# Kernel optimization log

Measured on AMD Instinct MI355X. Metric: run time of the kernel, lower is better.

Reference implementation:

```python
import jax, jax.numpy as jnp
import numpy as np
import math

LN_EPS = 1e-5
NORM_EPS = 1e-12


def _l2norm(v):
    # F.normalize(p=2, dim=-1): v / max(||v||, eps)
    n = jnp.sqrt(jnp.sum(v * v, axis=-1, keepdims=True))
    return v / jnp.maximum(n, NORM_EPS)


def setup_inputs() -> dict:
    key = jax.random.key(0)
    B, C, P, D, R = 64, 21, 96, 256, 32
    H = D // 4  # gate MLP hidden = 64
    ks = jax.random.split(key, 24)
    f32 = jnp.float32
    inp = {
        "x": jax.random.normal(ks[0], (B * C, P, D), dtype=f32),
        "ln_w": jnp.ones((D,), f32),
        "ln_b": jnp.zeros((D,), f32),
        "Wd": jax.random.normal(ks[1], (D, R), f32) / np.sqrt(D),
        "bd": jax.random.normal(ks[2], (R,), f32) * 0.02,
        "Wq": jax.random.normal(ks[3], (R, R), f32) / np.sqrt(R),
        "Wk": jax.random.normal(ks[4], (R, R), f32) / np.sqrt(R),
        "Wv": jax.random.normal(ks[5], (R, R), f32) / np.sqrt(R),
        "Wg": jax.random.normal(ks[6], (R, R), f32) / np.sqrt(R),
        "bg": jax.random.normal(ks[7], (R,), f32) * 0.02,
        "Wu": jax.random.normal(ks[8], (R, D), f32) / np.sqrt(R),
        "bu": jax.random.normal(ks[9], (D,), f32) * 0.02,
        "cn1_w": jax.random.normal(ks[10], (1, H), f32),
        "cn1_b": jax.random.normal(ks[11], (H,), f32) * 0.02,
        "cn2_w": jax.random.normal(ks[12], (H, D), f32) / np.sqrt(H),
        "cn2_b": jnp.full((D,), -5.0, f32),
        "dn1_w": jax.random.normal(ks[13], (D, H), f32) / np.sqrt(D),
        "dn1_b": jax.random.normal(ks[14], (H,), f32) * 0.02,
        "dn2_w": jax.random.normal(ks[15], (H, D), f32) / np.sqrt(H),
        "dn2_b": jax.random.normal(ks[16], (D,), f32) * 0.02,
        "epsilon": jnp.asarray(0.1, f32),
        "B": B,
        "C": C,
    }
    return inp


def reference(x, ln_w, ln_b, Wd, bd, Wq, Wk, Wv, Wg, bg, Wu, bu,
              cn1_w, cn1_b, cn2_w, cn2_b, dn1_w, dn1_b, dn2_w, dn2_b,
              epsilon, B, C):
    BC, P, D = x.shape
    gelu = lambda t: jax.nn.gelu(t, approximate=False)

    # [B*C,P,D] -> [B*P,C,D]: mix across channels per (batch, patch)
    h = x.reshape(B, C, P, D).transpose(0, 2, 1, 3).reshape(B * P, C, D)

    # LayerNorm over D
    mu = jnp.mean(h, axis=-1, keepdims=True)
    var = jnp.var(h, axis=-1, keepdims=True)
    h_norm = (h - mu) * jax.lax.rsqrt(var + LN_EPS) * ln_w + ln_b

    # bottleneck projection down to rank
    h_low = h_norm @ Wd + bd  # [BP, C, R]

    # Hydra attention: cosine-sim linear attention, global pool over C
    Q = _l2norm(h_low @ Wq)
    K = _l2norm(h_low @ Wk)
    V = h_low @ Wv
    global_feat = jnp.sum(K * V, axis=1, keepdims=True)  # [BP, 1, R]
    h_attn = Q * global_feat  # [BP, C, R]

    # content gate in low-rank space, then project up
    gate_c = jax.nn.sigmoid(h_low @ Wg + bg)
    mixed = (h_attn * gate_c) @ Wu + bu  # [BP, C, D]

    # AdaptiveGate (hybrid): channel MLP on log C + eps * data MLP on channel variance
    log_c = math.log(max(C, 2)) / math.log(1000.0)
    lc = jnp.full((1, 1), log_c, dtype=x.dtype)
    channel_logits = gelu(lc @ cn1_w + cn1_b) @ cn2_w + cn2_b  # [1, D]
    chan_var = jnp.var(h, axis=1, ddof=1)  # unbiased var over C -> [BP, D]
    data_corr = gelu(chan_var @ dn1_w + dn1_b) @ dn2_w + dn2_b  # [BP, D]
    gate_val = jax.nn.sigmoid(channel_logits + epsilon * data_corr)[:, None, :]

    out = h + gate_val * mixed  # [BP, C, D]
    return out.reshape(B, P, C, D).transpose(0, 2, 1, 3).reshape(BC, P, D)
```

## Files before the change

kernel.cpp:

```cpp
#include <hip/hip_runtime.h>
#include <math.h>


#define DD 256
#define CC 21
#define RR 32
#define HH 64
#define PP 96
#define BB 64
#define PD (PP * DD)
#define NBP (BB * PP)
#define NT 256

#define HBS 264
#define LWS 40

#define WS_WDB  0
#define WS_W4B  16384
#define WS_WUB  24576
#define WS_DN1P 40960
#define WS_DN2P 73728
#define WS_S1   106496
#define WS_S2   106624
#define WS_LG   106752

typedef __attribute__((ext_vector_type(8))) short bf16x8;
typedef __attribute__((ext_vector_type(4))) float f32x4;
typedef __attribute__((ext_vector_type(4))) unsigned short u16x4;

__device__ __forceinline__ float gelu_exact(float x) {
    return 0.5f * x * (1.0f + erff(x * 0.70710678118654752440f));
}
__device__ __forceinline__ float sigmoidf_(float x) {
    return 1.0f / (1.0f + __expf(-x));
}
__device__ __forceinline__ short f2bf(float f) {
    union { float f; unsigned u; } v; v.f = f;
    unsigned r = v.u + 0x7FFFu + ((v.u >> 16) & 1u);
    return (short)(unsigned short)(r >> 16);
}
__device__ __forceinline__ float bf2f_s(short s) {
    union { unsigned u; float f; } v; v.u = ((unsigned)(unsigned short)s) << 16;
    return v.f;
}

#define DPP_ADD(v, ctrl)                                                      \
    (v) += __builtin_bit_cast(float, __builtin_amdgcn_update_dpp(             \
               0, __builtin_bit_cast(int, (v)), (ctrl), 0xF, 0xF, true))

__device__ __forceinline__ float rowsum16(float v) {
    DPP_ADD(v, 0xB1);
    DPP_ADD(v, 0x4E);
    DPP_ADD(v, 0x124);
    DPP_ADD(v, 0x128);
    return v;
}
__device__ __forceinline__ float rdlane(float v, int l) {
    return __builtin_bit_cast(float,
        __builtin_amdgcn_readlane(__builtin_bit_cast(int, v), l));
}

extern "C" __global__ __launch_bounds__(NT)
void hydra_preproc(const float* __restrict__ ln_w, const float* __restrict__ ln_b,
                   const float* __restrict__ Wd,   const float* __restrict__ bd,
                   const float* __restrict__ Wq,   const float* __restrict__ Wk,
                   const float* __restrict__ Wv,   const float* __restrict__ Wg,
                   const float* __restrict__ Wu,
                   const float* __restrict__ cn1w, const float* __restrict__ cn1b,
                   const float* __restrict__ cn2w, const float* __restrict__ cn2b,
                   const float* __restrict__ dn1w, const float* __restrict__ dn2w,
                   short* __restrict__ WdB, short* __restrict__ W4B,
                   short* __restrict__ WuB, short* __restrict__ dn1P,
                   short* __restrict__ dn2P,
                   float* __restrict__ s1p, float* __restrict__ s2p,
                   float* __restrict__ logits)
{
    const int t = threadIdx.x, lane = t & 63, w = t >> 6, bid = blockIdx.x;
    const int q = lane >> 4, nl = lane & 15;

    if (bid < 4) {
        int tile = bid * 4 + w;
        int kb = tile >> 1, ni = tile & 1;
        int kbase = kb * 32 + q * 8;
        int n = ni * 16 + nl;
        bf16x8 o;
        #pragma unroll
        for (int j = 0; j < 8; ++j) {
            int k = kbase + j;
            o[j] = f2bf(ln_w[k] * Wd[k * RR + n]);
        }
        *(bf16x8*)(WdB + tile * 512 + lane * 8) = o;
    } else if (bid < 6) {
        int ni = (bid - 4) * 4 + w;
        int n = ni * 16 + nl;
        const float* Wsel = (n < 32) ? Wq : (n < 64) ? Wk : (n < 96) ? Wv : Wg;
        int nn = n & 31;
        bf16x8 o;
        #pragma unroll
        for (int j = 0; j < 8; ++j) o[j] = f2bf(Wsel[(q * 8 + j) * RR + nn]);
        *(bf16x8*)(W4B + ni * 512 + lane * 8) = o;
    } else if (bid < 10) {
        int ni = (bid - 6) * 4 + w;
        int n = ni * 16 + nl;
        bf16x8 o;
        #pragma unroll
        for (int j = 0; j < 8; ++j) o[j] = f2bf(Wu[(q * 8 + j) * DD + n]);
        *(bf16x8*)(WuB + ni * 512 + lane * 8) = o;
    } else if (bid == 10) {
        __shared__ float red1[8][33], red2[8][33];
        __shared__ float clh[HH];
        int r = t & 31, ks = t >> 5;
        float a1 = 0.f, a2 = 0.f;
        for (int k = ks * 32; k < ks * 32 + 32; ++k) {
            float wv = Wd[k * RR + r];
            a1 += bf2f_s(f2bf(ln_w[k] * wv));
            a2 += ln_b[k] * wv;
        }
        red1[ks][r] = a1; red2[ks][r] = a2;
        if (t < HH) {
            const float lc = 0.44073977f;
            clh[t] = gelu_exact(lc * cn1w[t] + cn1b[t]);
        }
        __syncthreads();
        if (t < RR) {
            float s1 = 0.f, s2 = 0.f;
            #pragma unroll
            for (int s = 0; s < 8; ++s) { s1 += red1[s][t]; s2 += red2[s][t]; }
            s1p[t] = s1;
            s2p[t] = s2 + bd[t];
        }
        float a = 0.f;
        #pragma unroll 8
        for (int j = 0; j < HH; ++j) a += clh[j] * cn2w[j * DD + t];
        logits[t] = a + cn2b[t];
    } else if (bid < 19) {
        int slot = (bid - 11) * 256 + t;
        int kb = slot >> 6, j = slot & 63;
        bf16x8 o;
        #pragma unroll
        for (int ki = 0; ki < 8; ++ki) o[ki] = f2bf(dn1w[(kb * 8 + ki) * HH + j]);
        *(bf16x8*)(dn1P + slot * 8) = o;
    } else {
        int slot = (bid - 19) * 256 + t;
        int jb = slot >> 8, d = slot & 255;
        bf16x8 o;
        #pragma unroll
        for (int ji = 0; ji < 8; ++ji) o[ji] = f2bf(dn2w[(jb * 8 + ji) * DD + d]);
        *(bf16x8*)(dn2P + slot * 8) = o;
    }
}

extern "C" __global__ __launch_bounds__(NT, 5)
void hydra_fused(const float* __restrict__ x,
                 const float* __restrict__ bg,   const float* __restrict__ bu,
                 const float* __restrict__ dn1b, const float* __restrict__ dn2b,
                 const float* __restrict__ eps_p,
                 const short* __restrict__ WdB,  const short* __restrict__ W4B,
                 const short* __restrict__ WuB,  const short* __restrict__ dn1P,
                 const short* __restrict__ dn2P,
                 const float* __restrict__ s1p,  const float* __restrict__ s2p,
                 const float* __restrict__ logits,
                 float* __restrict__ out)
{
    __shared__ __align__(16) short  hbf[CC * HBS];
    __shared__ __align__(16) short  lowbf[32 * LWS];
    __shared__ __align__(16) float  sh_cv[DD];
    __shared__ __align__(16) float2 murs[32];
    __shared__ __align__(16) float  dn1p[128];
    __shared__ __align__(16) float  sh_h1[HH];
    __shared__ __align__(16) float  gfp[64];
    __shared__ __align__(16) float  sh_gf[RR];
    __shared__ __align__(16) float  sh_gate[DD];

    const int t    = threadIdx.x;
    const int lane = t & 63;
    const int w    = t >> 6;
    const int quad = lane >> 4;
    const int nl   = lane & 15;
    const int bp = blockIdx.x;
    const int b  = bp / PP;
    const int p  = bp - b * PP;
    const float* xbase = x   + (size_t)b * CC * PD + (size_t)p * DD;
    float*       obase = out + (size_t)b * CC * PD + (size_t)p * DD;

    if (t >= 21 && t < 32) murs[t] = make_float2(0.f, 0.f);
    #pragma unroll
    for (int iter = 0; iter < 6; ++iter) {
        int c = iter * 4 + w;
        bool act = (c < CC);
        float4 v = make_float4(0.f, 0.f, 0.f, 0.f);
        if (act) v = *(const float4*)(xbase + (size_t)c * PD + lane * 4);
        if (act) {
            u16x4 u;
            u[0] = (unsigned short)f2bf(v.x); u[1] = (unsigned short)f2bf(v.y);
            u[2] = (unsigned short)f2bf(v.z); u[3] = (unsigned short)f2bf(v.w);
            *(u16x4*)(hbf + c * HBS + lane * 4) = u;
        }
        float s  = v.x + v.y + v.z + v.w;
        float s2 = v.x * v.x + v.y * v.y + v.z * v.z + v.w * v.w;
        s  = rowsum16(s);
        s2 = rowsum16(s2);
        float tot  = rdlane(s, 0)  + rdlane(s, 16)  + rdlane(s, 32)  + rdlane(s, 48);
        float tot2 = rdlane(s2, 0) + rdlane(s2, 16) + rdlane(s2, 32) + rdlane(s2, 48);
        if (act && lane == 0) {
            float mu  = tot * (1.0f / DD);
            float var = tot2 * (1.0f / DD) - mu * mu;
            murs[c] = make_float2(mu, rsqrtf(var + 1e-5f));
        }
    }
    __syncthreads();

    {
        float cs = 0.f, cs2 = 0.f;
        #pragma unroll
        for (int c = 0; c < CC; ++c) {
            float v = bf2f_s(hbf[c * HBS + t]);
            cs += v; cs2 += v * v;
        }
        sh_cv[t] = (cs2 - cs * cs * (1.0f / CC)) * (1.0f / (CC - 1));
    }
    {
        const int mi = w & 1, ni = w >> 1;
        const int m  = mi * 16 + nl;
        const int mc = (m < CC) ? m : (CC - 1);
        f32x4 acc = {0.f, 0.f, 0.f, 0.f};
        #pragma unroll
        for (int kb = 0; kb < 8; ++kb) {
            bf16x8 a  = *(const bf16x8*)(hbf + mc * HBS + kb * 32 + quad * 8);
            bf16x8 bw = *(const bf16x8*)(WdB + (kb * 2 + ni) * 512 + lane * 8);
            acc = __builtin_amdgcn_mfma_f32_16x16x32_bf16(a, bw, acc, 0, 0, 0);
        }
        const int colg = ni * 16 + nl;
        const float s1v = s1p[colg], s2v = s2p[colg];
        #pragma unroll
        for (int reg = 0; reg < 4; ++reg) {
            int rowg = mi * 16 + quad * 4 + reg;
            float2 mr = murs[rowg];
            float hl = mr.y * (acc[reg] - mr.x * s1v) + s2v;
            lowbf[rowg * LWS + colg] = f2bf(hl);
        }
    }
    __syncthreads();

    const int mi2 = w >> 1;
    float qg0[4], qg1[4];
    if ((w & 1) == 0) {
        const int m = mi2 * 16 + nl;
        bf16x8 a = *(const bf16x8*)(lowbf + m * LWS + quad * 8);
        f32x4 acc[8];
        #pragma unroll
        for (int i = 0; i < 8; ++i) {
            bf16x8 bw = *(const bf16x8*)(W4B + i * 512 + lane * 8);
            f32x4 z = {0.f, 0.f, 0.f, 0.f};
            acc[i] = __builtin_amdgcn_mfma_f32_16x16x32_bf16(a, bw, z, 0, 0, 0);
        }
        const float bg0 = bg[nl], bg1 = bg[16 + nl];
        float kv0 = 0.f, kv1 = 0.f;
        #pragma unroll
        for (int reg = 0; reg < 4; ++reg) {
            float q0 = acc[0][reg], q1 = acc[1][reg];
            float k0 = acc[2][reg], k1 = acc[3][reg];
            float q2 = rowsum16(q0 * q0 + q1 * q1);
            float k2 = rowsum16(k0 * k0 + k1 * k1);
            float qi = 1.0f / fmaxf(sqrtf(q2), 1e-12f);
            float ki = 1.0f / fmaxf(sqrtf(k2), 1e-12f);
            float g0 = sigmoidf_(acc[6][reg] + bg0);
            float g1 = sigmoidf_(acc[7][reg] + bg1);
            qg0[reg] = q0 * qi * g0;
            qg1[reg] = q1 * qi * g1;
            int rowg = mi2 * 16 + quad * 4 + reg;
            float msk = (rowg < CC) ? 1.0f : 0.0f;
            kv0 += msk * (k0 * ki * acc[4][reg]);
            kv1 += msk * (k1 * ki * acc[5][reg]);
        }
        kv0 += __shfl_xor(kv0, 16); kv0 += __shfl_xor(kv0, 32);
        kv1 += __shfl_xor(kv1, 16); kv1 += __shfl_xor(kv1, 32);
        if (quad == 0) {
            gfp[mi2 * 32 + nl]      = kv0;
            gfp[mi2 * 32 + 16 + nl] = kv1;
        }
    } else {
        const int half = w >> 1;
        float part = 0.f;
        #pragma unroll
        for (int i = 0; i < 16; ++i) {
            int kb = half * 16 + i;
            bf16x8 wv = *(const bf16x8*)(dn1P + (kb * 64 + lane) * 8);
            f32x4 c0 = *(const f32x4*)(sh_cv + kb * 8);
            f32x4 c1 = *(const f32x4*)(sh_cv + kb * 8 + 4);
            part += bf2f_s(wv[0]) * c0[0] + bf2f_s(wv[1]) * c0[1]
                  + bf2f_s(wv[2]) * c0[2] + bf2f_s(wv[3]) * c0[3]
                  + bf2f_s(wv[4]) * c1[0] + bf2f_s(wv[5]) * c1[1]
                  + bf2f_s(wv[6]) * c1[2] + bf2f_s(wv[7]) * c1[3];
        }
        dn1p[half * 64 + lane] = part;
    }
    __syncthreads();

    if (t < HH) sh_h1[t] = gelu_exact(dn1p[t] + dn1p[64 + t] + dn1b[t]);
    if (t < RR) sh_gf[t] = gfp[t] + gfp[32 + t];
    __syncthreads();

    {
        const float eps = eps_p[0];
        float a1 = 0.f;
        #pragma unroll
        for (int jb = 0; jb < 8; ++jb) {
            bf16x8 wv = *(const bf16x8*)(dn2P + (jb * 256 + t) * 8);
            f32x4 h0 = *(const f32x4*)(sh_h1 + jb * 8);
            f32x4 h1 = *(const f32x4*)(sh_h1 + jb * 8 + 4);
            a1 += bf2f_s(wv[0]) * h0[0] + bf2f_s(wv[1]) * h0[1]
                + bf2f_s(wv[2]) * h0[2] + bf2f_s(wv[3]) * h0[3]
                + bf2f_s(wv[4]) * h1[0] + bf2f_s(wv[5]) * h1[1]
                + bf2f_s(wv[6]) * h1[2] + bf2f_s(wv[7]) * h1[3];
        }
        sh_gate[t] = sigmoidf_(logits[t] + eps * (a1 + dn2b[t]));
    }
    if ((w & 1) == 0) {
        float gf0 = sh_gf[nl], gf1 = sh_gf[16 + nl];
        #pragma unroll
        for (int reg = 0; reg < 4; ++reg) {
            int rowg = mi2 * 16 + quad * 4 + reg;
            lowbf[rowg * LWS + nl]      = f2bf(qg0[reg] * gf0);
            lowbf[rowg * LWS + 16 + nl] = f2bf(qg1[reg] * gf1);
        }
    }
    __syncthreads();

    {
        const int mi = w & 1, nig = (w >> 1) * 8;
        const int m = mi * 16 + nl;
        bf16x8 a = *(const bf16x8*)(lowbf + m * LWS + quad * 8);
        #pragma unroll
        for (int i = 0; i < 8; ++i) {
            bf16x8 bw = *(const bf16x8*)(WuB + (nig + i) * 512 + lane * 8);
            f32x4 z = {0.f, 0.f, 0.f, 0.f};
            f32x4 acc = __builtin_amdgcn_mfma_f32_16x16x32_bf16(a, bw, z, 0, 0, 0);
            const int d   = (nig + i) * 16 + nl;
            const float gd  = sh_gate[d];
            const float bud = bu[d];
            #pragma unroll
            for (int reg = 0; reg < 4; ++reg) {
                int c = mi * 16 + quad * 4 + reg;
                if (c < CC) {
                    float hres = bf2f_s(hbf[c * HBS + d]);
                    obase[(size_t)c * PD + d] = hres + gd * (acc[reg] + bud);
                }
            }
        }
    }
}

extern "C" void kernel_launch(void* const* d_in, const int* in_sizes, int n_in,
                              void* d_out, int out_size, void* d_ws, size_t ws_size,
                              hipStream_t stream) {
    const float* x    = (const float*)d_in[0];
    const float* ln_w = (const float*)d_in[1];
    const float* ln_b = (const float*)d_in[2];
    const float* Wd   = (const float*)d_in[3];
    const float* bd   = (const float*)d_in[4];
    const float* Wq   = (const float*)d_in[5];
    const float* Wk   = (const float*)d_in[6];
    const float* Wv   = (const float*)d_in[7];
    const float* Wg   = (const float*)d_in[8];
    const float* bg   = (const float*)d_in[9];
    const float* Wu   = (const float*)d_in[10];
    const float* bu   = (const float*)d_in[11];
    const float* cn1w = (const float*)d_in[12];
    const float* cn1b = (const float*)d_in[13];
    const float* cn2w = (const float*)d_in[14];
    const float* cn2b = (const float*)d_in[15];
    const float* dn1w = (const float*)d_in[16];
    const float* dn1b = (const float*)d_in[17];
    const float* dn2w = (const float*)d_in[18];
    const float* dn2b = (const float*)d_in[19];
    const float* eps  = (const float*)d_in[20];
    float* out = (float*)d_out;

    char* ws = (char*)d_ws;
    short* WdB  = (short*)(ws + WS_WDB);
    short* W4B  = (short*)(ws + WS_W4B);
    short* WuB  = (short*)(ws + WS_WUB);
    short* dn1P = (short*)(ws + WS_DN1P);
    short* dn2P = (short*)(ws + WS_DN2P);
    float* s1p  = (float*)(ws + WS_S1);
    float* s2p  = (float*)(ws + WS_S2);
    float* lg   = (float*)(ws + WS_LG);

    hydra_preproc<<<27, NT, 0, stream>>>(ln_w, ln_b, Wd, bd, Wq, Wk, Wv, Wg, Wu,
                                         cn1w, cn1b, cn2w, cn2b, dn1w, dn2w,
                                         WdB, W4B, WuB, dn1P, dn2P, s1p, s2p, lg);
    hydra_fused<<<NBP, NT, 0, stream>>>(x, bg, bu, dn1b, dn2b, eps,
                                        WdB, W4B, WuB, dn1P, dn2P, s1p, s2p, lg,
                                        out);
}
```

Measured before the change: 350.6 us.

## Transpose MFMA operand roles so outputs write as contiguous vectorized float4 rows

Measured after the change: 323.5 us. 7.7% less time.

```diff
diff --git a/kernel.cpp b/kernel.cpp
--- a/kernel.cpp
+++ b/kernel.cpp
@@ -183,7 +183,6 @@
     const float* xbase = x   + (size_t)b * CC * PD + (size_t)p * DD;
     float*       obase = out + (size_t)b * CC * PD + (size_t)p * DD;
 
-    if (t >= 21 && t < 32) murs[t] = make_float2(0.f, 0.f);
     #pragma unroll
     for (int iter = 0; iter < 6; ++iter) {
         int c = iter * 4 + w;
@@ -215,30 +214,31 @@
         #pragma unroll
         for (int c = 0; c < CC; ++c) {
             float v = bf2f_s(hbf[c * HBS + t]);
-            cs += v; cs2 += v * v;
+            cs += v; cs2 = fmaf(v, v, cs2);
         }
         sh_cv[t] = (cs2 - cs * cs * (1.0f / CC)) * (1.0f / (CC - 1));
     }
     {
-        const int mi = w & 1, ni = w >> 1;
-        const int m  = mi * 16 + nl;
-        const int mc = (m < CC) ? m : (CC - 1);
+        const int mt = w & 1, ct = w >> 1;
+        const int c  = ct * 16 + nl;
+        const int c_rd = (c < CC) ? c : (CC - 1);
+        const int r0 = mt * 16 + quad * 4;
         f32x4 acc = {0.f, 0.f, 0.f, 0.f};
         #pragma unroll
         for (int kb = 0; kb < 8; ++kb) {
-            bf16x8 a  = *(const bf16x8*)(hbf + mc * HBS + kb * 32 + quad * 8);
-            bf16x8 bw = *(const bf16x8*)(WdB + (kb * 2 + ni) * 512 + lane * 8);
-            acc = __builtin_amdgcn_mfma_f32_16x16x32_bf16(a, bw, acc, 0, 0, 0);
-        }
-        const int colg = ni * 16 + nl;
-        const float s1v = s1p[colg], s2v = s2p[colg];
-        #pragma unroll
-        for (int reg = 0; reg < 4; ++reg) {
-            int rowg = mi * 16 + quad * 4 + reg;
-            float2 mr = murs[rowg];
-            float hl = mr.y * (acc[reg] - mr.x * s1v) + s2v;
-            lowbf[rowg * LWS + colg] = f2bf(hl);
-        }
+            bf16x8 bh = *(const bf16x8*)(hbf + c_rd * HBS + kb * 32 + quad * 8);
+            bf16x8 aw = *(const bf16x8*)(WdB + (kb * 2 + mt) * 512 + lane * 8);
+            acc = __builtin_amdgcn_mfma_f32_16x16x32_bf16(aw, bh, acc, 0, 0, 0);
+        }
+        const float2 mr = murs[c_rd];
+        const f32x4 s1v = *(const f32x4*)(s1p + r0);
+        const f32x4 s2v = *(const f32x4*)(s2p + r0);
+        u16x4 o;
+        #pragma unroll
+        for (int reg = 0; reg < 4; ++reg)
+            o[reg] = (unsigned short)f2bf(
+                mr.y * (acc[reg] - mr.x * s1v[reg]) + s2v[reg]);
+        *(u16x4*)(lowbf + c * LWS + r0) = o;
     }
     __syncthreads();
 
@@ -281,19 +281,19 @@
         }
     } else {
         const int half = w >> 1;
-        float part = 0.f;
+        float p0 = 0.f, p1 = 0.f;
         #pragma unroll
         for (int i = 0; i < 16; ++i) {
             int kb = half * 16 + i;
             bf16x8 wv = *(const bf16x8*)(dn1P + (kb * 64 + lane) * 8);
             f32x4 c0 = *(const f32x4*)(sh_cv + kb * 8);
             f32x4 c1 = *(const f32x4*)(sh_cv + kb * 8 + 4);
-            part += bf2f_s(wv[0]) * c0[0] + bf2f_s(wv[1]) * c0[1]
-                  + bf2f_s(wv[2]) * c0[2] + bf2f_s(wv[3]) * c0[3]
-                  + bf2f_s(wv[4]) * c1[0] + bf2f_s(wv[5]) * c1[1]
-                  + bf2f_s(wv[6]) * c1[2] + bf2f_s(wv[7]) * c1[3];
-        }
-        dn1p[half * 64 + lane] = part;
+            p0 += bf2f_s(wv[0]) * c0[0] + bf2f_s(wv[1]) * c0[1]
+                + bf2f_s(wv[2]) * c0[2] + bf2f_s(wv[3]) * c0[3];
+            p1 += bf2f_s(wv[4]) * c1[0] + bf2f_s(wv[5]) * c1[1]
+                + bf2f_s(wv[6]) * c1[2] + bf2f_s(wv[7]) * c1[3];
+        }
+        dn1p[half * 64 + lane] = p0 + p1;
     }
     __syncthreads();
 
@@ -303,18 +303,18 @@
 
     {
         const float eps = eps_p[0];
-        float a1 = 0.f;
+        float a0 = 0.f, a1 = 0.f;
         #pragma unroll
         for (int jb = 0; jb < 8; ++jb) {
             bf16x8 wv = *(const bf16x8*)(dn2P + (jb * 256 + t) * 8);
             f32x4 h0 = *(const f32x4*)(sh_h1 + jb * 8);
             f32x4 h1 = *(const f32x4*)(sh_h1 + jb * 8 + 4);
-            a1 += bf2f_s(wv[0]) * h0[0] + bf2f_s(wv[1]) * h0[1]
-                + bf2f_s(wv[2]) * h0[2] + bf2f_s(wv[3]) * h0[3]
-                + bf2f_s(wv[4]) * h1[0] + bf2f_s(wv[5]) * h1[1]
+            a0 += bf2f_s(wv[0]) * h0[0] + bf2f_s(wv[1]) * h0[1]
+                + bf2f_s(wv[2]) * h0[2] + bf2f_s(wv[3]) * h0[3];
+            a1 += bf2f_s(wv[4]) * h1[0] + bf2f_s(wv[5]) * h1[1]
                 + bf2f_s(wv[6]) * h1[2] + bf2f_s(wv[7]) * h1[3];
         }
-        sh_gate[t] = sigmoidf_(logits[t] + eps * (a1 + dn2b[t]));
+        sh_gate[t] = sigmoidf_(logits[t] + eps * (a0 + a1 + dn2b[t]));
     }
     if ((w & 1) == 0) {
         float gf0 = sh_gf[nl], gf1 = sh_gf[16 + nl];
@@ -328,24 +328,36 @@
     __syncthreads();
 
     {
-        const int mi = w & 1, nig = (w >> 1) * 8;
-        const int m = mi * 16 + nl;
-        bf16x8 a = *(const bf16x8*)(lowbf + m * LWS + quad * 8);
-        #pragma unroll
-        for (int i = 0; i < 8; ++i) {
-            bf16x8 bw = *(const bf16x8*)(WuB + (nig + i) * 512 + lane * 8);
+        bf16x8 bf0 = *(const bf16x8*)(lowbf + nl * LWS + quad * 8);
+        bf16x8 bf1 = *(const bf16x8*)(lowbf + (16 + nl) * LWS + quad * 8);
+        const int c0 = nl, c1 = 16 + nl;
+        #pragma unroll
+        for (int i = 0; i < 4; ++i) {
+            const int dt = w * 4 + i;
+            bf16x8 af = *(const bf16x8*)(WuB + dt * 512 + lane * 8);
             f32x4 z = {0.f, 0.f, 0.f, 0.f};
-            f32x4 acc = __builtin_amdgcn_mfma_f32_16x16x32_bf16(a, bw, z, 0, 0, 0);
-            const int d   = (nig + i) * 16 + nl;
-            const float gd  = sh_gate[d];
-            const float bud = bu[d];
-            #pragma unroll
-            for (int reg = 0; reg < 4; ++reg) {
-                int c = mi * 16 + quad * 4 + reg;
-                if (c < CC) {
-                    float hres = bf2f_s(hbf[c * HBS + d]);
-                    obase[(size_t)c * PD + d] = hres + gd * (acc[reg] + bud);
-                }
+            f32x4 a0 = __builtin_amdgcn_mfma_f32_16x16x32_bf16(af, bf0, z, 0, 0, 0);
+            f32x4 a1 = __builtin_amdgcn_mfma_f32_16x16x32_bf16(af, bf1, z, 0, 0, 0);
+            const int db = dt * 16 + quad * 4;
+            const f32x4 gd  = *(const f32x4*)(sh_gate + db);
+            const f32x4 bud = *(const f32x4*)(bu + db);
+            {
+                u16x4 h4 = *(const u16x4*)(hbf + c0 * HBS + db);
+                f32x4 o;
+                #pragma unroll
+                for (int reg = 0; reg < 4; ++reg)
+                    o[reg] = fmaf(gd[reg], a0[reg] + bud[reg],
+                                  bf2f_s((short)h4[reg]));
+                *(f32x4*)(obase + (size_t)c0 * PD + db) = o;
+            }
+            if (nl < CC - 16) {
+                u16x4 h4 = *(const u16x4*)(hbf + c1 * HBS + db);
+                f32x4 o;
+                #pragma unroll
+                for (int reg = 0; reg < 4; ++reg)
+                    o[reg] = fmaf(gd[reg], a1[reg] + bud[reg],
+                                  bf2f_s((short)h4[reg]));
+                *(f32x4*)(obase + (size_t)c1 * PD + db) = o;
             }
         }
     }
```
